# Kernel optimization log

Measured on AMD Instinct MI355X. Metric: run time of the kernel, lower is better.

The kernel has to match this reference:

```python
import jax, jax.numpy as jnp
import numpy as np

# Static tree structure: B jets, each a perfect binary tree of depth DEPTH.
B = 64
DEPTH = 12                       # levels 0..DEPTH; level j has B*2**j nodes
N_FEAT = 7
N_HID = 128
LEVEL_SIZES = [B * (1 << j) for j in range(DEPTH + 1)]
OFFSETS = np.concatenate([[0], np.cumsum(LEVEL_SIZES)]).astype(np.int64).tolist()
TOTAL = OFFSETS[-1]              # 524224 nodes
INNER_SIZES = LEVEL_SIZES[:-1]   # all nodes inner except leaf level
INNER_OFF = np.concatenate([[0], np.cumsum(INNER_SIZES)]).astype(np.int64).tolist()


def setup_inputs() -> dict:
    key = jax.random.key(0)
    k_c, k_wu, k_wh = jax.random.split(key, 3)
    contents = jax.random.normal(k_c, (TOTAL, N_FEAT), dtype=jnp.float32)
    # children: per level j < DEPTH, a random pairing (permutation) of level j+1 nodes
    rng = np.random.default_rng(0)
    ch = []
    for j in range(DEPTH):
        perm = rng.permutation(LEVEL_SIZES[j + 1]).astype(np.int32)
        ch.append(perm.reshape(LEVEL_SIZES[j], 2))
    children = jnp.asarray(np.concatenate(ch, axis=0))  # [262080, 2]
    # Learned params (torch nn.Linear: y = x @ W.T + b)
    w_u = jax.random.normal(k_wu, (N_HID, N_FEAT), dtype=jnp.float32) / np.float32(np.sqrt(N_FEAT))
    b_u = jnp.zeros((N_HID,), jnp.float32)
    w_h = jax.random.normal(k_wh, (N_HID, 3 * N_HID), dtype=jnp.float32) / np.float32(np.sqrt(3 * N_HID))
    b_h = jnp.zeros((N_HID,), jnp.float32)
    return {"contents": contents, "children": children,
            "w_u": w_u, "b_u": b_u, "w_h": w_h, "b_h": b_h}


def reference(contents, children, w_u, b_u, w_h, b_h):
    # Bottom-up pass over tree levels (leaves -> root), mirroring the torch loop
    # over levels[::-1]. Perfect binary tree: every non-leaf node is inner.
    emb = None
    for j in range(DEPTH, -1, -1):
        c_j = contents[OFFSETS[j]:OFFSETS[j + 1]]              # [B*2^j, F]
        u = jnp.tanh(c_j @ w_u.T + b_u)                        # [B*2^j, H]
        if j < DEPTH:
            ch_j = children[INNER_OFF[j]:INNER_OFF[j + 1]]     # [B*2^j, 2]
            h_L = emb[ch_j[:, 0]]                              # gather from prev level
            h_R = emb[ch_j[:, 1]]
            emb = jnp.tanh(jnp.concatenate([h_L, h_R, u], axis=1) @ w_h.T + b_h)
        else:
            emb = u  # leaf level: no inner nodes
    return emb.reshape(B, -1)  # root embedding per jet: [B, N_HID]
```

## Files before the change

### kernel.cpp

```cpp
#include <hip/hip_runtime.h>
#include <hip/hip_bf16.h>


#define NF 7
#define NH 128
#define XSTR 136
#define XSTR3 392

typedef __bf16 bf16;
typedef __bf16 bf16x8 __attribute__((ext_vector_type(8)));
typedef float floatx16 __attribute__((ext_vector_type(16)));
typedef float floatx2 __attribute__((ext_vector_type(2)));

__device__ __forceinline__ float ftanh(float x){
    float e = __builtin_amdgcn_exp2f(x * 2.8853900817779268f);
    return fmaf(-2.0f, __builtin_amdgcn_rcpf(e + 1.0f), 1.0f);
}

__device__ __forceinline__ floatx2 pkfma(float c, floatx2 w, floatx2 a){
    floatx2 cc = {c, c};
    return __builtin_elementwise_fma(cc, w, a);
}

__global__ __launch_bounds__(256) void k_prep0(
    const int2* __restrict__ children,
    const float* __restrict__ w_u, const float* __restrict__ b_u,
    const float* __restrict__ w_h,
    int* __restrict__ ids_A, int* __restrict__ ids_B,
    bf16* __restrict__ wb, bf16* __restrict__ w_ub)
{
    const int t = threadIdx.x;
    const int b = blockIdx.x;
    if (b < 4){
        int root = b * 256 + t;
        int* base = ids_A + root * 128;
        const int2* ch4 = children + 960;
        const int2* ch5 = children + 1984;
        const int2* ch6 = children + 4032;
        const int2* ch7 = children + 8128;
        const int2* ch8 = children + 16320;
        const int2* ch9 = children + 32704;
        int l5[2], l6[4], l7[8], l8[16], l9[32];
        { int2 c = ch4[root]; l5[0] = c.x; l5[1] = c.y; }
        #pragma unroll
        for (int k = 0; k < 2; ++k){ int2 c = ch5[l5[k]]; l6[2*k] = c.x; l6[2*k+1] = c.y; }
        #pragma unroll
        for (int k = 0; k < 4; ++k){ int2 c = ch6[l6[k]]; l7[2*k] = c.x; l7[2*k+1] = c.y; }
        #pragma unroll
        for (int k = 0; k < 8; ++k){ int2 c = ch7[l7[k]]; l8[2*k] = c.x; l8[2*k+1] = c.y; }
        #pragma unroll
        for (int k = 0; k < 16; ++k){ int2 c = ch8[l8[k]]; l9[2*k] = c.x; l9[2*k+1] = c.y; }
        base[0] = root;
        base[1] = l5[0]; base[2] = l5[1];
        #pragma unroll
        for (int k = 0; k < 4; ++k)  base[3 + k]  = l6[k];
        #pragma unroll
        for (int k = 0; k < 8; ++k)  base[7 + k]  = l7[k];
        #pragma unroll
        for (int k = 0; k < 16; ++k) base[15 + k] = l8[k];
        #pragma unroll
        for (int k = 0; k < 32; ++k) base[31 + k] = l9[k];
        #pragma unroll
        for (int k = 0; k < 32; ++k){
            int2 c = ch9[l9[k]];
            base[63 + 2*k] = c.x; base[64 + 2*k] = c.y;
        }
    } else if (b == 4){
        if (t < 64){
            int root = t;
            int* base = ids_B + root * 32;
            const int2* ch0 = children;
            const int2* ch1 = children + 64;
            const int2* ch2 = children + 192;
            const int2* ch3 = children + 448;
            int l1[2], l2[4], l3[8];
            { int2 c = ch0[root]; l1[0] = c.x; l1[1] = c.y; }
            #pragma unroll
            for (int k = 0; k < 2; ++k){ int2 c = ch1[l1[k]]; l2[2*k] = c.x; l2[2*k+1] = c.y; }
            #pragma unroll
            for (int k = 0; k < 4; ++k){ int2 c = ch2[l2[k]]; l3[2*k] = c.x; l3[2*k+1] = c.y; }
            base[0] = root;
            base[1] = l1[0]; base[2] = l1[1];
            #pragma unroll
            for (int k = 0; k < 4; ++k) base[3 + k] = l2[k];
            #pragma unroll
            for (int k = 0; k < 8; ++k) base[7 + k] = l3[k];
            #pragma unroll
            for (int k = 0; k < 8; ++k){
                int2 c = ch3[l3[k]];
                base[15 + 2*k] = c.x; base[16 + 2*k] = c.y;
            }
        } else if (t < 192){
            int col = t - 64;
            union { uint4 u4[2]; bf16 h[16]; } row;
            #pragma unroll
            for (int f = 0; f < NF; ++f) row.h[f] = (bf16)w_u[col * NF + f];
            row.h[7] = (bf16)b_u[col];
            #pragma unroll
            for (int k = 8; k < 16; ++k) row.h[k] = (bf16)0.0f;
            *(uint4*)&w_ub[col * 16]     = row.u4[0];
            *(uint4*)&w_ub[col * 16 + 8] = row.u4[1];
        }
    } else {
        int idx = (b - 5) * 256 + t;
        wb[idx] = (bf16)w_h[idx];
    }
}

__global__ __launch_bounds__(256, 2) void k_lvl11(
    const float* __restrict__ contents, const int2* __restrict__ children,
    const bf16* __restrict__ w_ub, const bf16* __restrict__ wb,
    const float* __restrict__ b_h, bf16* __restrict__ emb11)
{
    __shared__ bf16 xs[64 * XSTR3];
    __shared__ int chS[128];
    const int t = threadIdx.x;
    const int b = blockIdx.x;

    const int node0 = b * 64;
    const int2* ch11 = children + 131008;
    const float* cont11 = contents + (size_t)131008 * NF;
    const float* contL  = contents + (size_t)262080 * NF;

    if (t < 64){ int2 c = ch11[node0 + t]; chS[2*t] = c.x; chS[2*t + 1] = c.y; }

    const int lane = t & 63;
    const int ct = t >> 6;
    const int m = lane & 31;
    const int q = lane >> 5;
    const int colg = ct * 32 + m;
    const bf16x8 bu = *(const bf16x8*)(w_ub + (size_t)colg * 16 + q * 8);
    __syncthreads();

    float rows[6][NF];
    if (q == 0){
        #pragma unroll
        for (int tile = 0; tile < 6; ++tile){
            const float* src;
            if (tile < 4) src = contL + (size_t)chS[tile * 32 + m] * NF;
            else          src = cont11 + (size_t)(node0 + (tile - 4) * 32 + m) * NF;
            #pragma unroll
            for (int f = 0; f < NF; ++f) rows[tile][f] = src[f];
        }
    }

    #pragma unroll
    for (int tile = 0; tile < 6; ++tile){
        bf16x8 a = {bf16(0.f),bf16(0.f),bf16(0.f),bf16(0.f),
                    bf16(0.f),bf16(0.f),bf16(0.f),bf16(0.f)};
        if (q == 0){
            union { bf16x8 v; bf16 h[8]; } u8;
            #pragma unroll
            for (int f = 0; f < NF; ++f) u8.h[f] = (bf16)rows[tile][f];
            u8.h[7] = (bf16)1.0f;
            a = u8.v;
        }
        floatx16 acc = {0,0,0,0,0,0,0,0,0,0,0,0,0,0,0,0};
        acc = __builtin_amdgcn_mfma_f32_32x32x16_bf16(a, bu, acc, 0, 0, 0);
        #pragma unroll
        for (int r = 0; r < 16; ++r){
            int row = (r & 3) + 8 * (r >> 2) + 4 * q;
            bf16 hv = (bf16)ftanh(acc[r]);
            if (tile < 4){
                int c = tile * 32 + row;
                xs[(c >> 1) * XSTR3 + (c & 1) * 128 + colg] = hv;
            } else {
                int i = (tile - 4) * 32 + row;
                xs[i * XSTR3 + 256 + colg] = hv;
            }
        }
    }
    __syncthreads();

    floatx16 acc0 = {0,0,0,0,0,0,0,0,0,0,0,0,0,0,0,0};
    floatx16 acc1 = {0,0,0,0,0,0,0,0,0,0,0,0,0,0,0,0};
    const bf16* bq = wb + (size_t)colg * 384 + q * 8;
    const bf16* xa = &xs[m * XSTR3 + q * 8];
    #pragma unroll
    for (int grp = 0; grp < 3; ++grp){
        bf16x8 bfr[8];
        #pragma unroll
        for (int kk = 0; kk < 8; ++kk)
            bfr[kk] = *(const bf16x8*)(bq + grp * 128 + kk * 16);
        #pragma unroll
        for (int kk = 0; kk < 8; ++kk){
            bf16x8 a0 = *(const bf16x8*)(xa + grp * 128 + kk * 16);
            bf16x8 a1 = *(const bf16x8*)(xa + grp * 128 + kk * 16 + 32 * XSTR3);
            acc0 = __builtin_amdgcn_mfma_f32_32x32x16_bf16(a0, bfr[kk], acc0, 0, 0, 0);
            acc1 = __builtin_amdgcn_mfma_f32_32x32x16_bf16(a1, bfr[kk], acc1, 0, 0, 0);
        }
    }

    const float bv = b_h[colg];
    #pragma unroll
    for (int nt = 0; nt < 2; ++nt){
        const floatx16* accp = nt ? &acc1 : &acc0;
        #pragma unroll
        for (int r = 0; r < 16; ++r){
            int row  = (r & 3) + 8 * (r >> 2) + 4 * q;
            int node = node0 + nt * 32 + row;
            emb11[(size_t)node * NH + colg] = (bf16)ftanh((*accp)[r] + bv);
        }
    }
}

__global__ __launch_bounds__(256, 4) void k_inner(
    const int2* __restrict__ children, const float* __restrict__ contents,
    const float* __restrict__ w_u, const float* __restrict__ b_u,
    const bf16* __restrict__ wb, const float* __restrict__ b_h,
    const bf16* __restrict__ emb_next, bf16* __restrict__ out_b)
{
    __shared__ bf16 xs[64 * XSTR];
    __shared__ int2 ch_s[64];
    __shared__ float cs[64 * 8];
    const int t = threadIdx.x;
    const int block0 = blockIdx.x * 64;
    if (t < 64) ch_s[t] = children[block0 + t];
    if (t < 112){
        float4 v = ((const float4*)(contents + (size_t)block0 * NF))[t];
        int e = t * 4;
        float vv[4] = {v.x, v.y, v.z, v.w};
        #pragma unroll
        for (int r = 0; r < 4; ++r){ int ee = e + r; cs[(ee/7)*8 + (ee%7)] = vv[r]; }
    }
    const int cp = t & 63;
    const int quarter = t >> 6;
    floatx2 wu2[NF];
    {
        const float* w0 = w_u + (size_t)(2 * cp) * NF;
        #pragma unroll
        for (int f = 0; f < NF; ++f){ floatx2 w = {w0[f], w0[NF + f]}; wu2[f] = w; }
    }
    floatx2 bu2 = {b_u[2 * cp], b_u[2 * cp + 1]};
    const int lane = t & 63;
    const int ct = t >> 6;
    const int m = lane & 31;
    const int q = lane >> 5;
    floatx16 acc0 = {0,0,0,0,0,0,0,0,0,0,0,0,0,0,0,0};
    floatx16 acc1 = {0,0,0,0,0,0,0,0,0,0,0,0,0,0,0,0};
    const bf16* bq = wb + ((size_t)(ct * 32 + m) * 384 + q * 8);
    #pragma unroll 1
    for (int p = 0; p < 3; ++p){
        __syncthreads();
        if (p < 2){
            #pragma unroll
            for (int r = 0; r < 4; ++r){
                int task = r * 256 + t;
                int i = task >> 4, part = task & 15;
                int row = (p == 0) ? ch_s[i].x : ch_s[i].y;
                uint4 v = *(const uint4*)(emb_next + (size_t)row * NH + part * 8);
                *(uint4*)&xs[i * XSTR + part * 8] = v;
            }
        } else {
            #pragma unroll 4
            for (int i = 0; i < 16; ++i){
                int node = quarter * 16 + i;
                float4 c0 = *(const float4*)&cs[node * 8];
                float4 c1 = *(const float4*)&cs[node * 8 + 4];
                floatx2 a = bu2;
                a = pkfma(c0.x, wu2[0], a);
                a = pkfma(c0.y, wu2[1], a);
                a = pkfma(c0.z, wu2[2], a);
                a = pkfma(c0.w, wu2[3], a);
                a = pkfma(c1.x, wu2[4], a);
                a = pkfma(c1.y, wu2[5], a);
                a = pkfma(c1.z, wu2[6], a);
                union { unsigned int u; bf16 h[2]; } pk;
                pk.h[0] = (bf16)ftanh(a[0]);
                pk.h[1] = (bf16)ftanh(a[1]);
                ((unsigned int*)xs)[node * (XSTR / 2) + cp] = pk.u;
            }
        }
        bf16x8 bfr[8];
        #pragma unroll
        for (int kk = 0; kk < 8; ++kk)
            bfr[kk] = *(const bf16x8*)(bq + p * 128 + kk * 16);
        __syncthreads();
        const bf16* xa = &xs[m * XSTR + q * 8];
        #pragma unroll
        for (int kk = 0; kk < 8; ++kk){
            bf16x8 a0 = *(const bf16x8*)(xa + kk * 16);
            bf16x8 a1 = *(const bf16x8*)(xa + kk * 16 + 32 * XSTR);
            acc0 = __builtin_amdgcn_mfma_f32_32x32x16_bf16(a0, bfr[kk], acc0, 0, 0, 0);
            acc1 = __builtin_amdgcn_mfma_f32_32x32x16_bf16(a1, bfr[kk], acc1, 0, 0, 0);
        }
    }
    const int colg = ct * 32 + m;
    const float bv = b_h[colg];
    #pragma unroll
    for (int nt = 0; nt < 2; ++nt){
        const floatx16* accp = nt ? &acc1 : &acc0;
        #pragma unroll
        for (int r = 0; r < 16; ++r){
            int row  = (r & 3) + 8 * (r >> 2) + 4 * q;
            int node = block0 + nt * 32 + row;
            out_b[(size_t)node * NH + colg] = (bf16)ftanh((*accp)[r] + bv);
        }
    }
}

__global__ __launch_bounds__(256, 2) void k_tailA(
    const int* __restrict__ ids_A, const float* __restrict__ contents,
    const float* __restrict__ w_u, const float* __restrict__ b_u,
    const bf16* __restrict__ wb, const float* __restrict__ b_h,
    const bf16* __restrict__ emb10, bf16* __restrict__ emb4)
{
    __shared__ bf16 xs[32 * XSTR3];
    __shared__ bf16 embL[32 * 136];
    __shared__ int ids[128];
    const int t = threadIdx.x, root = blockIdx.x;
    const int ct = t >> 6, lane = t & 63, m = lane & 31, q = lane >> 5;
    const int cp = t & 63;
    const float bv = b_h[ct * 32 + m];
    if (t < 32) ((uint4*)ids)[t] = ((const uint4*)(ids_A + root * 128))[t];
    const bf16* bq = wb + ((size_t)(ct * 32 + m) * 384 + q * 8);

    floatx2 wu2[NF];
    {
        const float* w0 = w_u + (size_t)(2 * cp) * NF;
        #pragma unroll
        for (int f = 0; f < NF; ++f){ floatx2 w = {w0[f], w0[NF + f]}; wu2[f] = w; }
    }
    const floatx2 bu2 = {b_u[2 * cp], b_u[2 * cp + 1]};

    bf16x8 bfr[3][8];
    #pragma unroll
    for (int grp = 0; grp < 3; ++grp)
        #pragma unroll
        for (int kk = 0; kk < 8; ++kk)
            bfr[grp][kk] = *(const bf16x8*)(bq + grp * 128 + kk * 16);
    __syncthreads();

    #pragma unroll 1
    for (int l = 9; l >= 4; --l){
        const int n = 1 << (l - 4);
        #pragma unroll 1
        for (int r = 0; r < 4; ++r){
            int task = r * 256 + t;
            if (task < n * 32){
                int i = task >> 5, half = (task >> 4) & 1, part = task & 15;
                uint4 v;
                if (l == 9) v = *(const uint4*)(emb10 + (size_t)ids[63 + 2*i + half] * NH + part * 8);
                else        v = *(uint4*)&embL[(2*i + half) * 136 + part * 8];
                *(uint4*)&xs[i * XSTR3 + half * 128 + part * 8] = v;
            }
        }
        #pragma unroll 1
        for (int r = 0; r < 8; ++r){
            int task = r * 256 + t;
            if (task < n * 64){
                int i = task >> 6;
                size_t row = (size_t)64 * ((1u << l) - 1) + ids[(n - 1) + i];
                const float* src = contents + row * NF;
                floatx2 a = bu2;
                a = pkfma(src[0], wu2[0], a);
                a = pkfma(src[1], wu2[1], a);
                a = pkfma(src[2], wu2[2], a);
                a = pkfma(src[3], wu2[3], a);
                a = pkfma(src[4], wu2[4], a);
                a = pkfma(src[5], wu2[5], a);
                a = pkfma(src[6], wu2[6], a);
                union { unsigned int u; bf16 h[2]; } pk;
                pk.h[0] = (bf16)ftanh(a[0]);
                pk.h[1] = (bf16)ftanh(a[1]);
                *(unsigned int*)&xs[i * XSTR3 + 256 + 2 * cp] = pk.u;
            }
        }
        __syncthreads();
        floatx16 accs[3];
        #pragma unroll
        for (int g = 0; g < 3; ++g) accs[g] = (floatx16){0,0,0,0,0,0,0,0,0,0,0,0,0,0,0,0};
        const bf16* xa = &xs[m * XSTR3 + q * 8];
        #pragma unroll
        for (int grp = 0; grp < 3; ++grp){
            #pragma unroll
            for (int kk = 0; kk < 8; ++kk){
                bf16x8 a0 = *(const bf16x8*)(xa + grp * 128 + kk * 16);
                accs[grp] = __builtin_amdgcn_mfma_f32_32x32x16_bf16(a0, bfr[grp][kk], accs[grp], 0, 0, 0);
            }
        }
        floatx16 acc = accs[0] + accs[1] + accs[2];
        __syncthreads();
        #pragma unroll
        for (int r = 0; r < 16; ++r){
            int row = (r & 3) + 8 * (r >> 2) + 4 * q;
            if (row < n){
                float v = ftanh(acc[r] + bv);
                if (l > 4) embL[row * 136 + ct * 32 + m] = (bf16)v;
                else       emb4[(size_t)root * NH + ct * 32 + m] = (bf16)v;
            }
        }
        __syncthreads();
    }
}

__global__ __launch_bounds__(256, 2) void k_tailB(
    const int* __restrict__ ids_B, const float* __restrict__ contents,
    const float* __restrict__ w_u, const float* __restrict__ b_u,
    const bf16* __restrict__ wb, const float* __restrict__ b_h,
    const bf16* __restrict__ emb4, float* __restrict__ out_f)
{
    __shared__ bf16 xs[8 * XSTR3];
    __shared__ bf16 embL[8 * 136];
    __shared__ int ids[32];
    const int t = threadIdx.x, root = blockIdx.x;
    const int ct = t >> 6, lane = t & 63, m = lane & 31, q = lane >> 5;
    const int cp = t & 63;
    const float bv = b_h[ct * 32 + m];
    if (t < 8) ((uint4*)ids)[t] = ((const uint4*)(ids_B + root * 32))[t];
    const bf16* bq = wb + ((size_t)(ct * 32 + m) * 384 + q * 8);

    floatx2 wu2[NF];
    {
        const float* w0 = w_u + (size_t)(2 * cp) * NF;
        #pragma unroll
        for (int f = 0; f < NF; ++f){ floatx2 w = {w0[f], w0[NF + f]}; wu2[f] = w; }
    }
    const floatx2 bu2 = {b_u[2 * cp], b_u[2 * cp + 1]};

    bf16x8 bfr[3][8];
    #pragma unroll
    for (int grp = 0; grp < 3; ++grp)
        #pragma unroll
        for (int kk = 0; kk < 8; ++kk)
            bfr[grp][kk] = *(const bf16x8*)(bq + grp * 128 + kk * 16);
    __syncthreads();

    #pragma unroll 1
    for (int l = 3; l >= 0; --l){
        const int n = 1 << l;
        {
            int task = t;
            if (task < n * 32){
                int i = task >> 5, half = (task >> 4) & 1, part = task & 15;
                uint4 v;
                if (l == 3) v = *(const uint4*)(emb4 + (size_t)ids[15 + 2*i + half] * NH + part * 8);
                else        v = *(uint4*)&embL[(2*i + half) * 136 + part * 8];
                *(uint4*)&xs[i * XSTR3 + half * 128 + part * 8] = v;
            }
        }
        #pragma unroll 1
        for (int r = 0; r < 2; ++r){
            int task = r * 256 + t;
            if (task < n * 64){
                int i = task >> 6;
                size_t row = (size_t)64 * ((1u << l) - 1) + ids[(n - 1) + i];
                const float* src = contents + row * NF;
                floatx2 a = bu2;
                a = pkfma(src[0], wu2[0], a);
                a = pkfma(src[1], wu2[1], a);
                a = pkfma(src[2], wu2[2], a);
                a = pkfma(src[3], wu2[3], a);
                a = pkfma(src[4], wu2[4], a);
                a = pkfma(src[5], wu2[5], a);
                a = pkfma(src[6], wu2[6], a);
                union { unsigned int u; bf16 h[2]; } pk;
                pk.h[0] = (bf16)ftanh(a[0]);
                pk.h[1] = (bf16)ftanh(a[1]);
                *(unsigned int*)&xs[i * XSTR3 + 256 + 2 * cp] = pk.u;
            }
        }
        __syncthreads();
        floatx16 accs[3];
        #pragma unroll
        for (int g = 0; g < 3; ++g) accs[g] = (floatx16){0,0,0,0,0,0,0,0,0,0,0,0,0,0,0,0};
        const bf16* xa = &xs[m * XSTR3 + q * 8];
        #pragma unroll
        for (int grp = 0; grp < 3; ++grp){
            #pragma unroll
            for (int kk = 0; kk < 8; ++kk){
                bf16x8 a0 = *(const bf16x8*)(xa + grp * 128 + kk * 16);
                accs[grp] = __builtin_amdgcn_mfma_f32_32x32x16_bf16(a0, bfr[grp][kk], accs[grp], 0, 0, 0);
            }
        }
        floatx16 acc = accs[0] + accs[1] + accs[2];
        __syncthreads();
        #pragma unroll
        for (int r = 0; r < 16; ++r){
            int row = (r & 3) + 8 * (r >> 2) + 4 * q;
            if (row < n){
                float v = ftanh(acc[r] + bv);
                if (l > 0) embL[row * 136 + ct * 32 + m] = (bf16)v;
                else       out_f[(size_t)root * NH + ct * 32 + m] = v;
            }
        }
        __syncthreads();
    }
}

extern "C" void kernel_launch(void* const* d_in, const int* in_sizes, int n_in,
                              void* d_out, int out_size, void* d_ws, size_t ws_size,
                              hipStream_t stream){
    const float* contents = (const float*)d_in[0];
    const int2*  children = (const int2*)d_in[1];
    const float* w_u      = (const float*)d_in[2];
    const float* b_u      = (const float*)d_in[3];
    const float* w_h      = (const float*)d_in[4];
    const float* b_h      = (const float*)d_in[5];
    float* outf = (float*)d_out;

    bf16* embA    = (bf16*)d_ws;
    bf16* embB    = embA + (size_t)65536 * NH;
    bf16* wb      = embB + (size_t)131072 * NH;
    int*  ids_A   = (int*)(wb + (size_t)NH * 384);
    int*  ids_B   = ids_A + 1024 * 128;
    bf16* w_ub    = (bf16*)(ids_B + 64 * 32);

    hipLaunchKernelGGL(k_prep0, dim3(197), dim3(256), 0, stream,
                       children, w_u, b_u, w_h, ids_A, ids_B, wb, w_ub);
    hipLaunchKernelGGL(k_lvl11, dim3(2048), dim3(256), 0, stream,
                       contents, children, w_ub, wb, b_h, embB);
    hipLaunchKernelGGL(k_inner, dim3(1024), dim3(256), 0, stream,
                       children + 65472, contents + (size_t)65472 * NF,
                       w_u, b_u, wb, b_h, embB, embA);
    hipLaunchKernelGGL(k_tailA, dim3(1024), dim3(256), 0, stream,
                       ids_A, contents, w_u, b_u, wb, b_h, embA, embB);
    hipLaunchKernelGGL(k_tailB, dim3(64), dim3(256), 0, stream,
                       ids_B, contents, w_u, b_u, wb, b_h, embB, outf);
}
```

Baseline: 210.5 us.

## Precompute all tail-level leaf projections up front into shared memory

```diff
diff --git a/kernel.cpp b/kernel.cpp
--- a/kernel.cpp
+++ b/kernel.cpp
@@ -6,6 +6,8 @@
 #define NH 128
 #define XSTR 136
 #define XSTR3 392
+#define XS2 264
+#define USTR 136
 
 typedef __bf16 bf16;
 typedef __bf16 bf16x8 __attribute__((ext_vector_type(8)));
@@ -305,8 +307,9 @@
     const bf16* __restrict__ wb, const float* __restrict__ b_h,
     const bf16* __restrict__ emb10, bf16* __restrict__ emb4)
 {
-    __shared__ bf16 xs[32 * XSTR3];
+    __shared__ bf16 xs[32 * XS2];
     __shared__ bf16 embL[32 * 136];
+    __shared__ bf16 u_all[63 * USTR];
     __shared__ int ids[128];
     const int t = threadIdx.x, root = blockIdx.x;
     const int ct = t >> 6, lane = t & 63, m = lane & 31, q = lane >> 5;
@@ -331,53 +334,68 @@
             bfr[grp][kk] = *(const bf16x8*)(bq + grp * 128 + kk * 16);
     __syncthreads();
 
+    #pragma unroll
+    for (int r = 0; r < 4; ++r){
+        int task = r * 256 + t;
+        int i = task >> 5, half = (task >> 4) & 1, part = task & 15;
+        uint4 v = *(const uint4*)(emb10 + (size_t)ids[63 + 2*i + half] * NH + part * 8);
+        *(uint4*)&xs[i * XS2 + half * 128 + part * 8] = v;
+    }
+    #pragma unroll
+    for (int r = 0; r < 16; ++r){
+        int task = r * 256 + t;
+        if (task < 4032){
+            int j = task >> 6;
+            int k = 31 - __clz(j + 1);
+            size_t row = ((size_t)1024 << k) - 64 + ids[j];
+            const float* src = contents + row * NF;
+            floatx2 a = bu2;
+            a = pkfma(src[0], wu2[0], a);
+            a = pkfma(src[1], wu2[1], a);
+            a = pkfma(src[2], wu2[2], a);
+            a = pkfma(src[3], wu2[3], a);
+            a = pkfma(src[4], wu2[4], a);
+            a = pkfma(src[5], wu2[5], a);
+            a = pkfma(src[6], wu2[6], a);
+            union { unsigned int u; bf16 h[2]; } pk;
+            pk.h[0] = (bf16)ftanh(a[0]);
+            pk.h[1] = (bf16)ftanh(a[1]);
+            *(unsigned int*)&u_all[j * USTR + 2 * cp] = pk.u;
+        }
+    }
+    __syncthreads();
+
     #pragma unroll 1
     for (int l = 9; l >= 4; --l){
         const int n = 1 << (l - 4);
-        #pragma unroll 1
-        for (int r = 0; r < 4; ++r){
-            int task = r * 256 + t;
-            if (task < n * 32){
-                int i = task >> 5, half = (task >> 4) & 1, part = task & 15;
-                uint4 v;
-                if (l == 9) v = *(const uint4*)(emb10 + (size_t)ids[63 + 2*i + half] * NH + part * 8);
-                else        v = *(uint4*)&embL[(2*i + half) * 136 + part * 8];
-                *(uint4*)&xs[i * XSTR3 + half * 128 + part * 8] = v;
-            }
-        }
-        #pragma unroll 1
-        for (int r = 0; r < 8; ++r){
-            int task = r * 256 + t;
-            if (task < n * 64){
-                int i = task >> 6;
-                size_t row = (size_t)64 * ((1u << l) - 1) + ids[(n - 1) + i];
-                const float* src = contents + row * NF;
-                floatx2 a = bu2;
-                a = pkfma(src[0], wu2[0], a);
-                a = pkfma(src[1], wu2[1], a);
-                a = pkfma(src[2], wu2[2], a);
-                a = pkfma(src[3], wu2[3], a);
-                a = pkfma(src[4], wu2[4], a);
-                a = pkfma(src[5], wu2[5], a);
-                a = pkfma(src[6], wu2[6], a);
-                union { unsigned int u; bf16 h[2]; } pk;
-                pk.h[0] = (bf16)ftanh(a[0]);
-                pk.h[1] = (bf16)ftanh(a[1]);
-                *(unsigned int*)&xs[i * XSTR3 + 256 + 2 * cp] = pk.u;
-            }
-        }
-        __syncthreads();
+        if (l < 9){
+            #pragma unroll
+            for (int r = 0; r < 2; ++r){
+                int task = r * 256 + t;
+                if (task < n * 32){
+                    int i = task >> 5, half = (task >> 4) & 1, part = task & 15;
+                    *(uint4*)&xs[i * XS2 + half * 128 + part * 8] =
+                        *(uint4*)&embL[(2*i + half) * 136 + part * 8];
+                }
+            }
+            __syncthreads();
+        }
         floatx16 accs[3];
         #pragma unroll
         for (int g = 0; g < 3; ++g) accs[g] = (floatx16){0,0,0,0,0,0,0,0,0,0,0,0,0,0,0,0};
-        const bf16* xa = &xs[m * XSTR3 + q * 8];
-        #pragma unroll
-        for (int grp = 0; grp < 3; ++grp){
+        const bf16* xa  = &xs[m * XS2 + q * 8];
+        const bf16* xau = &u_all[((n - 1) + m) * USTR + q * 8];
+        #pragma unroll
+        for (int g = 0; g < 2; ++g)
             #pragma unroll
             for (int kk = 0; kk < 8; ++kk){
-                bf16x8 a0 = *(const bf16x8*)(xa + grp * 128 + kk * 16);
-                accs[grp] = __builtin_amdgcn_mfma_f32_32x32x16_bf16(a0, bfr[grp][kk], accs[grp], 0, 0, 0);
-            }
+                bf16x8 a0 = *(const bf16x8*)(xa + g * 128 + kk * 16);
+                accs[g] = __builtin_amdgcn_mfma_f32_32x32x16_bf16(a0, bfr[g][kk], accs[g], 0, 0, 0);
+            }
+        #pragma unroll
+        for (int kk = 0; kk < 8; ++kk){
+            bf16x8 a0 = *(const bf16x8*)(xau + kk * 16);
+            accs[2] = __builtin_amdgcn_mfma_f32_32x32x16_bf16(a0, bfr[2][kk], accs[2], 0, 0, 0);
         }
         floatx16 acc = accs[0] + accs[1] + accs[2];
         __syncthreads();
@@ -400,8 +418,9 @@
     const bf16* __restrict__ wb, const float* __restrict__ b_h,
     const bf16* __restrict__ emb4, float* __restrict__ out_f)
 {
-    __shared__ bf16 xs[8 * XSTR3];
+    __shared__ bf16 xs[8 * XS2];
     __shared__ bf16 embL[8 * 136];
+    __shared__ bf16 u_all[16 * USTR];
     __shared__ int ids[32];
     const int t = threadIdx.x, root = blockIdx.x;
     const int ct = t >> 6, lane = t & 63, m = lane & 31, q = lane >> 5;
@@ -426,52 +445,63 @@
             bfr[grp][kk] = *(const bf16x8*)(bq + grp * 128 + kk * 16);
     __syncthreads();
 
+    {
+        int i = t >> 5, half = (t >> 4) & 1, part = t & 15;
+        uint4 v = *(const uint4*)(emb4 + (size_t)ids[15 + 2*i + half] * NH + part * 8);
+        *(uint4*)&xs[i * XS2 + half * 128 + part * 8] = v;
+    }
+    #pragma unroll
+    for (int r = 0; r < 4; ++r){
+        int task = r * 256 + t;
+        if (task < 960){
+            int j = task >> 6;
+            int k = 31 - __clz(j + 1);
+            size_t row = ((size_t)64 << k) - 64 + ids[j];
+            const float* src = contents + row * NF;
+            floatx2 a = bu2;
+            a = pkfma(src[0], wu2[0], a);
+            a = pkfma(src[1], wu2[1], a);
+            a = pkfma(src[2], wu2[2], a);
+            a = pkfma(src[3], wu2[3], a);
+            a = pkfma(src[4], wu2[4], a);
+            a = pkfma(src[5], wu2[5], a);
+            a = pkfma(src[6], wu2[6], a);
+            union { unsigned int u; bf16 h[2]; } pk;
+            pk.h[0] = (bf16)ftanh(a[0]);
+            pk.h[1] = (bf16)ftanh(a[1]);
+            *(unsigned int*)&u_all[j * USTR + 2 * cp] = pk.u;
+        }
+    }
+    __syncthreads();
+
     #pragma unroll 1
     for (int l = 3; l >= 0; --l){
         const int n = 1 << l;
-        {
+        if (l < 3){
             int task = t;
             if (task < n * 32){
                 int i = task >> 5, half = (task >> 4) & 1, part = task & 15;
-                uint4 v;
-                if (l == 3) v = *(const uint4*)(emb4 + (size_t)ids[15 + 2*i + half] * NH + part * 8);
-                else        v = *(uint4*)&embL[(2*i + half) * 136 + part * 8];
-                *(uint4*)&xs[i * XSTR3 + half * 128 + part * 8] = v;
-            }
-        }
-        #pragma unroll 1
-        for (int r = 0; r < 2; ++r){
-            int task = r * 256 + t;
-            if (task < n * 64){
-                int i = task >> 6;
-                size_t row = (size_t)64 * ((1u << l) - 1) + ids[(n - 1) + i];
-                const float* src = contents + row * NF;
-                floatx2 a = bu2;
-                a = pkfma(src[0], wu2[0], a);
-                a = pkfma(src[1], wu2[1], a);
-                a = pkfma(src[2], wu2[2], a);
-                a = pkfma(src[3], wu2[3], a);
-                a = pkfma(src[4], wu2[4], a);
-                a = pkfma(src[5], wu2[5], a);
-                a = pkfma(src[6], wu2[6], a);
-                union { unsigned int u; bf16 h[2]; } pk;
-                pk.h[0] = (bf16)ftanh(a[0]);
-                pk.h[1] = (bf16)ftanh(a[1]);
-                *(unsigned int*)&xs[i * XSTR3 + 256 + 2 * cp] = pk.u;
-            }
-        }
-        __syncthreads();
+                *(uint4*)&xs[i * XS2 + half * 128 + part * 8] =
+                    *(uint4*)&embL[(2*i + half) * 136 + part * 8];
+            }
+            __syncthreads();
+        }
         floatx16 accs[3];
         #pragma unroll
         for (int g = 0; g < 3; ++g) accs[g] = (floatx16){0,0,0,0,0,0,0,0,0,0,0,0,0,0,0,0};
-        const bf16* xa = &xs[m * XSTR3 + q * 8];
-        #pragma unroll
-        for (int grp = 0; grp < 3; ++grp){
+        const bf16* xa  = &xs[(m & 7) * XS2 + q * 8];
+        const bf16* xau = &u_all[(((n - 1) + m) & 15) * USTR + q * 8];
+        #pragma unroll
+        for (int g = 0; g < 2; ++g)
             #pragma unroll
             for (int kk = 0; kk < 8; ++kk){
-                bf16x8 a0 = *(const bf16x8*)(xa + grp * 128 + kk * 16);
-                accs[grp] = __builtin_amdgcn_mfma_f32_32x32x16_bf16(a0, bfr[grp][kk], accs[grp], 0, 0, 0);
-            }
+                bf16x8 a0 = *(const bf16x8*)(xa + g * 128 + kk * 16);
+                accs[g] = __builtin_amdgcn_mfma_f32_32x32x16_bf16(a0, bfr[g][kk], accs[g], 0, 0, 0);
+            }
+        #pragma unroll
+        for (int kk = 0; kk < 8; ++kk){
+            bf16x8 a0 = *(const bf16x8*)(xau + kk * 16);
+            accs[2] = __builtin_amdgcn_mfma_f32_32x32x16_bf16(a0, bfr[2][kk], accs[2], 0, 0, 0);
         }
         floatx16 acc = accs[0] + accs[1] + accs[2];
         __syncthreads();
```

Result: faster. 198.5 us (-5.7%).
